# Optimization experiments

Hardware: AMD Instinct MI355X
Metric: run time of the kernel (lower is better)

The kernel has to match this reference:

```python
import jax, jax.numpy as jnp
import numpy as np

B, S, D = 2, 2048, 1024
H_Q, H_KV, DK, DV = 16, 8, 64, 64
R = H_Q // H_KV  # q heads per kv head (GQA)
THETA = 10000.0


def setup_inputs() -> dict:
    key = jax.random.key(0)
    ks = jax.random.split(key, 12)
    inv_freq = 1.0 / (THETA ** (jnp.arange(0, DK, 2, dtype=jnp.float32) / DK))  # [DK/2]
    angles = jnp.arange(S, dtype=jnp.float32)[:, None] * inv_freq[None, :]      # [S, DK/2]
    scale = 0.02
    return {
        "x": jax.random.normal(ks[0], (B, S, D), jnp.float32),
        "Wq": jax.random.normal(ks[1], (D, H_Q * DK), jnp.float32) * scale,
        "bq": jnp.zeros((H_Q * DK,), jnp.float32),
        "Wk": jax.random.normal(ks[2], (D, H_KV * DK), jnp.float32) * scale,
        "bk": jnp.zeros((H_KV * DK,), jnp.float32),
        "Wv": jax.random.normal(ks[3], (D, H_KV * DV), jnp.float32) * scale,
        "bv": jnp.zeros((H_KV * DV,), jnp.float32),
        "Wo": jax.random.normal(ks[4], (H_Q * DV, D), jnp.float32) * scale,
        "bo": jnp.zeros((D,), jnp.float32),
        "freqs_cos": jnp.cos(angles),
        "freqs_sin": jnp.sin(angles),
        "attention_mask": jax.random.bernoulli(ks[5], 0.9, (B, S)),  # True = real token
    }


def _rope(t, cos, sin):
    # t: [B, S, H, Dh]; cos/sin: [S, Dh/2]. Complex rotation on interleaved pairs.
    tp = t.reshape(*t.shape[:-1], -1, 2)
    x1, x2 = tp[..., 0], tp[..., 1]
    c = cos[None, :, None, :]
    s = sin[None, :, None, :]
    o1 = x1 * c - x2 * s
    o2 = x1 * s + x2 * c
    return jnp.stack([o1, o2], axis=-1).reshape(t.shape)


def reference(x, Wq, bq, Wk, bk, Wv, bv, Wo, bo, freqs_cos, freqs_sin, attention_mask):
    b, s, _ = x.shape
    q = (x @ Wq + bq).reshape(b, s, H_Q, DK)
    k = (x @ Wk + bk).reshape(b, s, H_KV, DK)
    v = (x @ Wv + bv).reshape(b, s, H_KV, DV)
    q = _rope(q, freqs_cos, freqs_sin)
    k = _rope(k, freqs_cos, freqs_sin)
    q = q.transpose(0, 2, 1, 3)                      # [B, Hq, S, DK]
    k = jnp.repeat(k.transpose(0, 2, 1, 3), R, axis=1)  # GQA expand -> [B, Hq, S, DK]
    v = jnp.repeat(v.transpose(0, 2, 1, 3), R, axis=1)  # [B, Hq, S, DV]
    causal = jnp.tril(jnp.ones((s, s), dtype=bool))
    # Module does logical_or(padding, causal) -- replicated faithfully.
    mask = jnp.logical_or(attention_mask[:, None, None, :], causal[None, None])
    scale = 1.0 / jnp.sqrt(jnp.float32(DK))
    scores = jnp.einsum('bhqd,bhkd->bhqk', q, k) * scale
    scores = jnp.where(mask, scores, -jnp.inf)
    attn = jax.nn.softmax(scores, axis=-1)
    out = jnp.einsum('bhqk,bhkd->bhqd', attn, v)
    out = out.transpose(0, 2, 1, 3).reshape(b, s, H_Q * DV)
    return out @ Wo + bo
```

## Files before the change

### kernel.cpp

```cpp
#include <hip/hip_runtime.h>
#include <hip/hip_bf16.h>
#include <math.h>

typedef __attribute__((ext_vector_type(8))) short bf16x8;
typedef __attribute__((ext_vector_type(4))) float f32x4;

#define OFF_XB  0ull
#define OFF_WT  (8ull<<20)
#define OFF_WO  (12ull<<20)
#define OFF_QB  (14ull<<20)
#define OFF_KB  (22ull<<20)
#define OFF_VT  (26ull<<20)
#define OFF_AO  (30ull<<20)
#define OFF_MB  (38ull<<20)

#define QSCALE 0.18033688056680276f

__device__ inline unsigned pack_bf162(float a, float b) {
    __hip_bfloat162 t = __float22bfloat162_rn(make_float2(a, b));
    return *(unsigned*)&t;
}

__device__ inline float exp2_fast(float x) {
    float r;
    asm("v_exp_f32 %0, %1" : "=v"(r) : "v"(x));
    return r;
}

__device__ inline void gload16(const void* g, void* l) {
    __builtin_amdgcn_global_load_lds(
        (const __attribute__((address_space(1))) void*)g,
        (__attribute__((address_space(3))) void*)l, 16, 0, 0);
}

__launch_bounds__(256)
__global__ void prep_kernel(const float* __restrict__ x,
                            const float* __restrict__ Wq, const float* __restrict__ Wk,
                            const float* __restrict__ Wv, const float* __restrict__ Wo,
                            const void* __restrict__ mraw,
                            __hip_bfloat16* __restrict__ XB,
                            __hip_bfloat16* __restrict__ WT,
                            __hip_bfloat16* __restrict__ WoT,
                            float* __restrict__ mbias) {
    __shared__ float T[32][33];
    __shared__ int bad01, badf;
    const int tid = threadIdx.x;
    const int bid = blockIdx.x;
    if (bid < 1024) {
        const int base = bid * 4096;
#pragma unroll
        for (int i = 0; i < 4; ++i) {
            const int e = base + (i * 256 + tid) * 4;
            const float4 v = *(const float4*)&x[e];
            uint2 pk;
            pk.x = pack_bf162(v.x, v.y);
            pk.y = pack_bf162(v.z, v.w);
            *(uint2*)&XB[e] = pk;
        }
    } else if (bid < 4096) {
        const float* src; int ldn, nbase; __hip_bfloat16* dst; int n0, k0;
        if (bid < 3072) {
            const int tb = bid - 1024;
            const int kt = tb >> 6, nt = tb & 63;
            n0 = nt * 32; k0 = kt * 32; dst = WT;
            if (n0 < 1024)      { src = Wq; ldn = 1024; nbase = n0; }
            else if (n0 < 1536) { src = Wk; ldn = 512;  nbase = n0 - 1024; }
            else                { src = Wv; ldn = 512;  nbase = n0 - 1536; }
        } else {
            const int tb = bid - 3072;
            const int kt = tb >> 5, nt = tb & 31;
            n0 = nt * 32; k0 = kt * 32; dst = WoT;
            src = Wo; ldn = 1024; nbase = n0;
        }
        const int c = tid & 31, r0 = tid >> 5;
#pragma unroll
        for (int i = 0; i < 4; ++i)
            T[r0 + 8 * i][c] = src[(size_t)(k0 + r0 + 8 * i) * ldn + nbase + c];
        __syncthreads();
#pragma unroll
        for (int i = 0; i < 4; ++i) {
            const int nn = r0 + 8 * i;
            dst[(size_t)(n0 + nn) * 1024 + k0 + c] = __float2bfloat16(T[c][nn]);
        }
    } else {
        if (tid == 0) { bad01 = 0; badf = 0; }
        __syncthreads();
        const unsigned* w = (const unsigned*)mraw;
#pragma unroll
        for (int i = 0; i < 4; ++i) {
            const unsigned v = w[tid * 4 + i];
            if (v > 1u) atomicAdd(&bad01, 1);
            if (v != 0u && v != 0x3F800000u) atomicAdd(&badf, 1);
        }
        __syncthreads();
        const int fmt = (bad01 == 0) ? 0 : ((badf == 0) ? 1 : 2);
        for (int i = tid; i < 4096; i += 256) {
            bool on;
            if (fmt == 2) on = (((const unsigned char*)mraw)[i] != 0);
            else          on = (w[i] != 0u);
            mbias[i] = on ? 0.f : -1e30f;
        }
    }
}

#define QSTAGE(SEL, K0_) do {                                                    \
    _Pragma("unroll") for (int rnd_ = 0; rnd_ < 4; ++rnd_) {                     \
        const int off_ = rnd_ * 4096 + wid * 1024 + lane * 16;                   \
        const int row_ = off_ >> 7;                                              \
        const int ch_  = ((off_ >> 4) & 7) ^ (row_ & 7);                         \
        gload16((const char*)Ag + ((size_t)(n0 + row_) * 1024 + (K0_) + ch_ * 8) * 2, \
                Asm + (SEL) * 16384 + rnd_ * 4096 + wid * 1024);                 \
        gload16((const char*)Bg + ((size_t)(m0 + row_) * 1024 + (K0_) + ch_ * 8) * 2, \
                Bsm + (SEL) * 16384 + rnd_ * 4096 + wid * 1024);                 \
    }                                                                            \
} while (0)

__launch_bounds__(256)
__global__ void qkv_mfma_kernel(const __hip_bfloat16* __restrict__ XB,
                                const __hip_bfloat16* __restrict__ WT,
                                const float* __restrict__ bq, const float* __restrict__ bk,
                                const float* __restrict__ bv,
                                const float* __restrict__ fc, const float* __restrict__ fs,
                                __hip_bfloat16* __restrict__ QB,
                                __hip_bfloat16* __restrict__ KB,
                                __hip_bfloat16* __restrict__ VT) {
    __shared__ __attribute__((aligned(16))) char Asm[32768];
    __shared__ __attribute__((aligned(16))) char Bsm[32768];
    const int tid = threadIdx.x;
    const int lane = tid & 63, wid = tid >> 6;
    const int c = lane & 15, g = lane >> 4;
    const int n0 = blockIdx.x * 128, m0 = blockIdx.y * 128;
    const int wn = (wid >> 1) * 64, wm = (wid & 1) * 64;
    const __hip_bfloat16* Ag = WT;
    const __hip_bfloat16* Bg = XB;

    f32x4 acc[4][4];
#pragma unroll
    for (int ni = 0; ni < 4; ++ni)
#pragma unroll
        for (int mj = 0; mj < 4; ++mj) acc[ni][mj] = f32x4{0.f, 0.f, 0.f, 0.f};

    QSTAGE(0, 0);
    int cur = 0;
    for (int kt = 0; kt < 16; ++kt) {
        const int k0 = kt * 64;
        if (kt < 15) {
            QSTAGE(cur ^ 1, k0 + 64);
            asm volatile("s_waitcnt vmcnt(8)" ::: "memory");
        } else {
            asm volatile("s_waitcnt vmcnt(0)" ::: "memory");
        }
        __builtin_amdgcn_sched_barrier(0);
        __builtin_amdgcn_s_barrier();
        __builtin_amdgcn_sched_barrier(0);

        const char* Ac = Asm + cur * 16384;
        const char* Bc = Bsm + cur * 16384;
#pragma unroll
        for (int ks = 0; ks < 2; ++ks) {
            bf16x8 af[4], bfr[4];
#pragma unroll
            for (int t = 0; t < 4; ++t) {
                const int sl = ((g + 4 * ks) ^ (c & 7)) << 4;
                af[t]  = *(const bf16x8*)(Ac + (wn + 16 * t + c) * 128 + sl);
                bfr[t] = *(const bf16x8*)(Bc + (wm + 16 * t + c) * 128 + sl);
            }
#pragma unroll
            for (int ni = 0; ni < 4; ++ni)
#pragma unroll
                for (int mj = 0; mj < 4; ++mj)
                    acc[ni][mj] = __builtin_amdgcn_mfma_f32_16x16x32_bf16(
                        af[ni], bfr[mj], acc[ni][mj], 0, 0, 0);
        }
        __builtin_amdgcn_sched_barrier(0);
        __builtin_amdgcn_s_barrier();
        __builtin_amdgcn_sched_barrier(0);
        cur ^= 1;
    }

#pragma unroll
    for (int ni = 0; ni < 4; ++ni) {
        const int nb = n0 + wn + 16 * ni + 4 * g;
        const float* bias; int nloc;
        if (nb < 1024)      { bias = bq; nloc = nb; }
        else if (nb < 1536) { bias = bk; nloc = nb - 1024; }
        else                { bias = bv; nloc = nb - 1536; }
        const float4 b4 = *(const float4*)&bias[nloc];
        const int h = nloc >> 6, dk = nb & 63;
#pragma unroll
        for (int mj = 0; mj < 4; ++mj) {
            const int tok = m0 + wm + 16 * mj + c;
            const int bb = tok >> 11, sp = tok & 2047;
            float v0 = acc[ni][mj][0] + b4.x;
            float v1 = acc[ni][mj][1] + b4.y;
            float v2 = acc[ni][mj][2] + b4.z;
            float v3 = acc[ni][mj][3] + b4.w;
            if (nb < 1536) {
                const int p = sp * 32 + (dk >> 1);
                const float c0 = fc[p], s0 = fs[p];
                const float c1 = fc[p + 1], s1 = fs[p + 1];
                float o0 = v0 * c0 - v1 * s0, o1 = v0 * s0 + v1 * c0;
                float o2 = v2 * c1 - v3 * s1, o3 = v2 * s1 + v3 * c1;
                uint2 pk;
                if (nb < 1024) {
                    o0 *= QSCALE; o1 *= QSCALE; o2 *= QSCALE; o3 *= QSCALE;
                    pk.x = pack_bf162(o0, o1); pk.y = pack_bf162(o2, o3);
                    *(uint2*)&QB[(size_t)((bb * 16 + h) * 2048 + sp) * 64 + dk] = pk;
                } else {
                    pk.x = pack_bf162(o0, o1); pk.y = pack_bf162(o2, o3);
                    *(uint2*)&KB[(size_t)((bb * 8 + h) * 2048 + sp) * 64 + dk] = pk;
                }
            } else {
                const size_t vb = (size_t)((bb * 8 + h) * 64 + dk) * 2048 + sp;
                VT[vb]          = __float2bfloat16(v0);
                VT[vb + 2048]   = __float2bfloat16(v1);
                VT[vb + 4096]   = __float2bfloat16(v2);
                VT[vb + 6144]   = __float2bfloat16(v3);
            }
        }
    }
}

__launch_bounds__(256)
__global__ void out_mfma_kernel(const __hip_bfloat16* __restrict__ AOB,
                                const __hip_bfloat16* __restrict__ WoT,
                                const float* __restrict__ bo,
                                float* __restrict__ out) {
    __shared__ __attribute__((aligned(16))) char Asm[32768];
    __shared__ __attribute__((aligned(16))) char Bsm[32768];
    const int tid = threadIdx.x;
    const int lane = tid & 63, wid = tid >> 6;
    const int c = lane & 15, g = lane >> 4;
    const int n0 = blockIdx.x * 128, m0 = blockIdx.y * 128;
    const int wn = (wid >> 1) * 64, wm = (wid & 1) * 64;
    const __hip_bfloat16* Ag = WoT;
    const __hip_bfloat16* Bg = AOB;

    f32x4 acc[4][4];
#pragma unroll
    for (int ni = 0; ni < 4; ++ni)
#pragma unroll
        for (int mj = 0; mj < 4; ++mj) acc[ni][mj] = f32x4{0.f, 0.f, 0.f, 0.f};

    QSTAGE(0, 0);
    int cur = 0;
    for (int kt = 0; kt < 16; ++kt) {
        const int k0 = kt * 64;
        if (kt < 15) {
            QSTAGE(cur ^ 1, k0 + 64);
            asm volatile("s_waitcnt vmcnt(8)" ::: "memory");
        } else {
            asm volatile("s_waitcnt vmcnt(0)" ::: "memory");
        }
        __builtin_amdgcn_sched_barrier(0);
        __builtin_amdgcn_s_barrier();
        __builtin_amdgcn_sched_barrier(0);

        const char* Ac = Asm + cur * 16384;
        const char* Bc = Bsm + cur * 16384;
#pragma unroll
        for (int ks = 0; ks < 2; ++ks) {
            bf16x8 af[4], bfr[4];
#pragma unroll
            for (int t = 0; t < 4; ++t) {
                const int sl = ((g + 4 * ks) ^ (c & 7)) << 4;
                af[t]  = *(const bf16x8*)(Ac + (wn + 16 * t + c) * 128 + sl);
                bfr[t] = *(const bf16x8*)(Bc + (wm + 16 * t + c) * 128 + sl);
            }
#pragma unroll
            for (int ni = 0; ni < 4; ++ni)
#pragma unroll
                for (int mj = 0; mj < 4; ++mj)
                    acc[ni][mj] = __builtin_amdgcn_mfma_f32_16x16x32_bf16(
                        af[ni], bfr[mj], acc[ni][mj], 0, 0, 0);
        }
        __builtin_amdgcn_sched_barrier(0);
        __builtin_amdgcn_s_barrier();
        __builtin_amdgcn_sched_barrier(0);
        cur ^= 1;
    }
#pragma unroll
    for (int ni = 0; ni < 4; ++ni) {
        const int nb = n0 + wn + 16 * ni + 4 * g;
        const float4 b4 = *(const float4*)&bo[nb];
#pragma unroll
        for (int mj = 0; mj < 4; ++mj) {
            const int tok = m0 + wm + 16 * mj + c;
            const f32x4 a = acc[ni][mj];
            const float4 st = make_float4(a[0] + b4.x, a[1] + b4.y,
                                          a[2] + b4.z, a[3] + b4.w);
            *(float4*)&out[(size_t)tok * 1024 + nb] = st;
        }
    }
}


#define STAGE128(SEL, K0_) do {                                                  \
    _Pragma("unroll") for (int rnd_ = 0; rnd_ < 4; ++rnd_) {                     \
        const int off_ = rnd_ * 4096 + wid * 1024 + lane * 16;                   \
        const int kr_ = off_ >> 7;                                               \
        const int kc_ = ((off_ >> 4) & 7) ^ (kr_ & 7);                           \
        gload16(Kh + (size_t)((K0_) + kr_) * 64 + kc_ * 8,                       \
                Ksm + (SEL) * 16384 + rnd_ * 4096 + wid * 1024);                 \
        const int vr_ = off_ >> 8;                                               \
        const int vc_ = ((off_ >> 4) & 15) ^ (vr_ & 15);                         \
        gload16(Vh + (size_t)vr_ * 2048 + (K0_) + vc_ * 8,                       \
                Vsm + (SEL) * 16384 + rnd_ * 4096 + wid * 1024);                 \
    }                                                                            \
} while (0)

__launch_bounds__(256, 2)
__global__ void attn_kernel(const __hip_bfloat16* __restrict__ QB,
                            const __hip_bfloat16* __restrict__ KB,
                            const __hip_bfloat16* __restrict__ VT,
                            const float* __restrict__ maskb,
                            __hip_bfloat16* __restrict__ AOB) {
    __shared__ __attribute__((aligned(16))) char Ksm[32768];
    __shared__ __attribute__((aligned(16))) char Vsm[32768];
    __shared__ char P_lds[4][4096];

    const int tid  = threadIdx.x;
    const int lane = tid & 63, wid = tid >> 6;
    const int c = lane & 15, g = lane >> 4;

    const int bid = blockIdx.x;
    const int o_  = (bid & 7) * 64 + (bid >> 3);
    const int qx = o_ & 15, h = (o_ >> 4) & 15, b = o_ >> 8;
    const int qb = qx * 128 + wid * 32;

    const __hip_bfloat16* Qh = QB + (size_t)(b * 16 + h)       * 2048 * 64;
    const __hip_bfloat16* Kh = KB + (size_t)(b * 8 + (h >> 1)) * 2048 * 64;
    const __hip_bfloat16* Vh = VT + (size_t)(b * 8 + (h >> 1)) * 64 * 2048;
    const float* mb = maskb + b * 2048;

    STAGE128(0, 0);

    bf16x8 bq[2][2];
#pragma unroll
    for (int rt = 0; rt < 2; ++rt)
#pragma unroll
        for (int ks = 0; ks < 2; ++ks)
            bq[rt][ks] = *(const bf16x8*)&Qh[(size_t)(qb + 16 * rt + c) * 64
                                             + 32 * ks + 8 * g];
    __syncthreads();

    const short oneb = (short)0x3F80;
    const bf16x8 ones = {oneb, oneb, oneb, oneb, oneb, oneb, oneb, oneb};

    f32x4 o[2][4];
    f32x4 lacc[2];
#pragma unroll
    for (int rt = 0; rt < 2; ++rt) {
        lacc[rt] = f32x4{0.f, 0.f, 0.f, 0.f};
#pragma unroll
        for (int mt = 0; mt < 4; ++mt) o[rt][mt] = f32x4{0.f, 0.f, 0.f, 0.f};
    }
    float m_[2] = {-INFINITY, -INFINITY};

    char* Pr = &P_lds[wid][0] + c * 256;
    const int swz = (c & 7) << 4;

    int cur = 0;
    for (int kt = 0; kt < 16; ++kt) {
        const int k0 = kt * 128;
        if (kt < 15) {
            STAGE128(cur ^ 1, k0 + 128);
            asm volatile("s_waitcnt vmcnt(8)" ::: "memory");
        } else {
            asm volatile("s_waitcnt vmcnt(0)" ::: "memory");
        }
        __builtin_amdgcn_sched_barrier(0);
        __builtin_amdgcn_s_barrier();
        __builtin_amdgcn_sched_barrier(0);

        const char* Kc = Ksm + cur * 16384;
        const char* Vc = Vsm + cur * 16384;

        const bool needb = (k0 + 127 > qb);
        f32x4 bv4[8];
        if (needb) {
#pragma unroll
            for (int mt = 0; mt < 8; ++mt)
                bv4[mt] = *(const f32x4*)&mb[k0 + 16 * mt + 4 * g];
        }

        f32x4 st[2][8];
        __builtin_amdgcn_s_setprio(1);
#pragma unroll
        for (int hf = 0; hf < 2; ++hf) {
            bf16x8 ak[4][2];
#pragma unroll
            for (int mt = 0; mt < 4; ++mt)
#pragma unroll
                for (int ks = 0; ks < 2; ++ks)
                    ak[mt][ks] = *(const bf16x8*)(Kc + (64 * hf + 16 * mt + c) * 128
                                                  + (((g + 4 * ks) ^ (c & 7)) << 4));
#pragma unroll
            for (int rt = 0; rt < 2; ++rt)
#pragma unroll
                for (int mt = 0; mt < 4; ++mt) {
                    f32x4 z = f32x4{0.f, 0.f, 0.f, 0.f};
                    z = __builtin_amdgcn_mfma_f32_16x16x32_bf16(ak[mt][0], bq[rt][0], z, 0, 0, 0);
                    z = __builtin_amdgcn_mfma_f32_16x16x32_bf16(ak[mt][1], bq[rt][1], z, 0, 0, 0);
                    st[rt][4 * hf + mt] = z;
                }
        }
        __builtin_amdgcn_s_setprio(0);

#pragma unroll
        for (int rt = 0; rt < 2; ++rt) {
            const int qw = qb + 16 * rt;
            if (k0 + 127 <= qw) {
            } else if (k0 > qw + 15) {
#pragma unroll
                for (int mt = 0; mt < 8; ++mt)
                    st[rt][mt] = st[rt][mt] + bv4[mt];
            } else {
                const int qg = qw + c;
#pragma unroll
                for (int mt = 0; mt < 8; ++mt)
#pragma unroll
                    for (int r = 0; r < 4; ++r) {
                        const int kg = k0 + 16 * mt + 4 * g + r;
                        st[rt][mt][r] += (kg <= qg) ? 0.f : bv4[mt][r];
                    }
            }
            const f32x4 a0 = __builtin_elementwise_max(st[rt][0], st[rt][1]);
            const f32x4 a1 = __builtin_elementwise_max(st[rt][2], st[rt][3]);
            const f32x4 a2 = __builtin_elementwise_max(st[rt][4], st[rt][5]);
            const f32x4 a3 = __builtin_elementwise_max(st[rt][6], st[rt][7]);
            const f32x4 b0 = __builtin_elementwise_max(a0, a1);
            const f32x4 b1 = __builtin_elementwise_max(a2, a3);
            const f32x4 mv = __builtin_elementwise_max(b0, b1);
            float pmax = fmaxf(fmaxf(mv[0], mv[1]), fmaxf(mv[2], mv[3]));
            pmax = fmaxf(pmax, __shfl_xor(pmax, 16));
            pmax = fmaxf(pmax, __shfl_xor(pmax, 32));
            if (!__all(pmax <= m_[rt] + 11.5f)) {
                const float mn = fmaxf(m_[rt], pmax);
                const float alpha = exp2_fast(m_[rt] - mn);
                m_[rt] = mn;
                lacc[rt][0] *= alpha;
#pragma unroll
                for (int mt = 0; mt < 4; ++mt) o[rt][mt] *= alpha;
            }
            const float mneg = m_[rt];
            const f32x4 m4 = {mneg, mneg, mneg, mneg};
#pragma unroll
            for (int mt = 0; mt < 8; ++mt) {
                const f32x4 e = st[rt][mt] - m4;
#pragma unroll
                for (int r = 0; r < 4; ++r)
                    st[rt][mt][r] = exp2_fast(e[r]);
            }

#pragma unroll
            for (int mt = 0; mt < 8; ++mt) {
                const unsigned w0 = pack_bf162(st[rt][mt][0], st[rt][mt][1]);
                const unsigned w1 = pack_bf162(st[rt][mt][2], st[rt][mt][3]);
                *(unsigned long long*)(Pr + ((32 * mt + 8 * g) ^ swz)) =
                    (unsigned long long)w0 | ((unsigned long long)w1 << 32);
            }

            __builtin_amdgcn_s_setprio(1);
#pragma unroll
            for (int ks = 0; ks < 4; ++ks) {
                const bf16x8 pb = *(const bf16x8*)(Pr + ((64 * ks + 16 * g) ^ swz));
                bf16x8 av[4];
#pragma unroll
                for (int mt = 0; mt < 4; ++mt)
                    av[mt] = *(const bf16x8*)(Vc + (16 * mt + c) * 256
                                              + (((4 * ks + g) ^ (c & 15)) << 4));
#pragma unroll
                for (int mt = 0; mt < 4; ++mt)
                    o[rt][mt] = __builtin_amdgcn_mfma_f32_16x16x32_bf16(av[mt], pb, o[rt][mt], 0, 0, 0);
                lacc[rt] = __builtin_amdgcn_mfma_f32_16x16x32_bf16(ones, pb, lacc[rt], 0, 0, 0);
            }
            __builtin_amdgcn_s_setprio(0);
        }

        __builtin_amdgcn_sched_barrier(0);
        __builtin_amdgcn_s_barrier();
        __builtin_amdgcn_sched_barrier(0);
        cur ^= 1;
    }

#pragma unroll
    for (int rt = 0; rt < 2; ++rt) {
        const float inv = 1.f / lacc[rt][0];
        const size_t tok = (size_t)(b * 2048 + qb + 16 * rt + c);
#pragma unroll
        for (int mt = 0; mt < 4; ++mt) {
            uint2 pk;
            pk.x = pack_bf162(o[rt][mt][0] * inv, o[rt][mt][1] * inv);
            pk.y = pack_bf162(o[rt][mt][2] * inv, o[rt][mt][3] * inv);
            *(uint2*)&AOB[tok * 1024 + h * 64 + 16 * mt + 4 * g] = pk;
        }
    }
}

extern "C" void kernel_launch(void* const* d_in, const int* in_sizes, int n_in,
                              void* d_out, int out_size, void* d_ws, size_t ws_size,
                              hipStream_t stream) {
    const float* x  = (const float*)d_in[0];
    const float* Wq = (const float*)d_in[1];
    const float* bq = (const float*)d_in[2];
    const float* Wk = (const float*)d_in[3];
    const float* bk = (const float*)d_in[4];
    const float* Wv = (const float*)d_in[5];
    const float* bv = (const float*)d_in[6];
    const float* Wo = (const float*)d_in[7];
    const float* bo = (const float*)d_in[8];
    const float* fc = (const float*)d_in[9];
    const float* fs = (const float*)d_in[10];
    const void*  am = d_in[11];

    char* ws = (char*)d_ws;
    __hip_bfloat16* XB  = (__hip_bfloat16*)(ws + OFF_XB);
    __hip_bfloat16* WT  = (__hip_bfloat16*)(ws + OFF_WT);
    __hip_bfloat16* WoT = (__hip_bfloat16*)(ws + OFF_WO);
    __hip_bfloat16* QB  = (__hip_bfloat16*)(ws + OFF_QB);
    __hip_bfloat16* KB  = (__hip_bfloat16*)(ws + OFF_KB);
    __hip_bfloat16* VT  = (__hip_bfloat16*)(ws + OFF_VT);
    __hip_bfloat16* AOB = (__hip_bfloat16*)(ws + OFF_AO);
    float* mbias = (float*)(ws + OFF_MB);
    float* out   = (float*)d_out;

    hipLaunchKernelGGL(prep_kernel, dim3(4097), dim3(256), 0, stream,
                       x, Wq, Wk, Wv, Wo, am, XB, WT, WoT, mbias);
    hipLaunchKernelGGL(qkv_mfma_kernel, dim3(16, 32), dim3(256), 0, stream,
                       XB, WT, bq, bk, bv, fc, fs, QB, KB, VT);
    hipLaunchKernelGGL(attn_kernel, dim3(512), dim3(256), 0, stream,
                       QB, KB, VT, mbias, AOB);
    hipLaunchKernelGGL(out_mfma_kernel, dim3(8, 32), dim3(256), 0, stream,
                       AOB, WoT, bo, out);
}
```

Measured before the change: 132.0 us.

## Software-pipeline attention so QK of next tile overlaps softmax/PV of previous

```diff
diff --git a/kernel.cpp b/kernel.cpp
--- a/kernel.cpp
+++ b/kernel.cpp
@@ -295,17 +295,105 @@
 }
 
 
-#define STAGE128(SEL, K0_) do {                                                  \
+#define STAGE_K(SEL, T_) do {                                                    \
+    const int sk0_ = (T_) * 128;                                                 \
     _Pragma("unroll") for (int rnd_ = 0; rnd_ < 4; ++rnd_) {                     \
         const int off_ = rnd_ * 4096 + wid * 1024 + lane * 16;                   \
         const int kr_ = off_ >> 7;                                               \
         const int kc_ = ((off_ >> 4) & 7) ^ (kr_ & 7);                           \
-        gload16(Kh + (size_t)((K0_) + kr_) * 64 + kc_ * 8,                       \
+        gload16(Kh + (size_t)(sk0_ + kr_) * 64 + kc_ * 8,                        \
                 Ksm + (SEL) * 16384 + rnd_ * 4096 + wid * 1024);                 \
+    }                                                                            \
+} while (0)
+
+#define STAGE_V(SEL, T_) do {                                                    \
+    const int sv0_ = (T_) * 128;                                                 \
+    _Pragma("unroll") for (int rnd_ = 0; rnd_ < 4; ++rnd_) {                     \
+        const int off_ = rnd_ * 4096 + wid * 1024 + lane * 16;                   \
         const int vr_ = off_ >> 8;                                               \
         const int vc_ = ((off_ >> 4) & 15) ^ (vr_ & 15);                         \
-        gload16(Vh + (size_t)vr_ * 2048 + (K0_) + vc_ * 8,                       \
+        gload16(Vh + (size_t)vr_ * 2048 + sv0_ + vc_ * 8,                        \
                 Vsm + (SEL) * 16384 + rnd_ * 4096 + wid * 1024);                 \
+    }                                                                            \
+} while (0)
+
+#define SOFTMAX_PV(PT, VC_) do {                                                 \
+    const int kp0_ = (PT) * 128;                                                 \
+    _Pragma("unroll") for (int rt = 0; rt < 2; ++rt) {                           \
+        const int qw_ = qb + 16 * rt;                                            \
+        if (kp0_ + 127 <= qw_) {                                                 \
+        } else if (kp0_ > qw_ + 15) {                                            \
+            _Pragma("unroll") for (int mt = 0; mt < 8; ++mt)                     \
+                stp[rt][mt] = stp[rt][mt] + bv4[mt];                             \
+        } else {                                                                 \
+            const int qg_ = qw_ + c;                                             \
+            _Pragma("unroll") for (int mt = 0; mt < 8; ++mt)                     \
+            _Pragma("unroll") for (int r = 0; r < 4; ++r) {                      \
+                const int kg_ = kp0_ + 16 * mt + 4 * g + r;                      \
+                stp[rt][mt][r] += (kg_ <= qg_) ? 0.f : bv4[mt][r];               \
+            }                                                                    \
+        }                                                                        \
+        const f32x4 a0_ = __builtin_elementwise_max(stp[rt][0], stp[rt][1]);     \
+        const f32x4 a1_ = __builtin_elementwise_max(stp[rt][2], stp[rt][3]);     \
+        const f32x4 a2_ = __builtin_elementwise_max(stp[rt][4], stp[rt][5]);     \
+        const f32x4 a3_ = __builtin_elementwise_max(stp[rt][6], stp[rt][7]);     \
+        const f32x4 b0_ = __builtin_elementwise_max(a0_, a1_);                   \
+        const f32x4 b1_ = __builtin_elementwise_max(a2_, a3_);                   \
+        const f32x4 mv_ = __builtin_elementwise_max(b0_, b1_);                   \
+        float pmax = fmaxf(fmaxf(mv_[0], mv_[1]), fmaxf(mv_[2], mv_[3]));        \
+        pmax = fmaxf(pmax, __shfl_xor(pmax, 16));                                \
+        pmax = fmaxf(pmax, __shfl_xor(pmax, 32));                                \
+        if (!__all(pmax <= m_[rt] + 11.5f)) {                                    \
+            const float mn_ = fmaxf(m_[rt], pmax);                               \
+            const float alpha_ = exp2_fast(m_[rt] - mn_);                        \
+            m_[rt] = mn_;                                                        \
+            lacc[rt][0] *= alpha_;                                               \
+            _Pragma("unroll") for (int mt = 0; mt < 4; ++mt) o[rt][mt] *= alpha_;\
+        }                                                                        \
+        const f32x4 m4_ = {m_[rt], m_[rt], m_[rt], m_[rt]};                      \
+        _Pragma("unroll") for (int mt = 0; mt < 8; ++mt) {                       \
+            const f32x4 e_ = stp[rt][mt] - m4_;                                  \
+            _Pragma("unroll") for (int r = 0; r < 4; ++r)                        \
+                stp[rt][mt][r] = exp2_fast(e_[r]);                               \
+        }                                                                        \
+        _Pragma("unroll") for (int mt = 0; mt < 8; ++mt) {                       \
+            const unsigned w0_ = pack_bf162(stp[rt][mt][0], stp[rt][mt][1]);     \
+            const unsigned w1_ = pack_bf162(stp[rt][mt][2], stp[rt][mt][3]);     \
+            *(unsigned long long*)(Pr + ((32 * mt + 8 * g) ^ swz)) =             \
+                (unsigned long long)w0_ | ((unsigned long long)w1_ << 32);       \
+        }                                                                        \
+        _Pragma("unroll") for (int ks = 0; ks < 4; ++ks) {                       \
+            const bf16x8 pb_ = *(const bf16x8*)(Pr + ((64 * ks + 16 * g) ^ swz));\
+            bf16x8 av_[4];                                                       \
+            _Pragma("unroll") for (int mt = 0; mt < 4; ++mt)                     \
+                av_[mt] = *(const bf16x8*)((VC_) + (16 * mt + c) * 256           \
+                                           + (((4 * ks + g) ^ (c & 15)) << 4));  \
+            _Pragma("unroll") for (int mt = 0; mt < 4; ++mt)                     \
+                o[rt][mt] = __builtin_amdgcn_mfma_f32_16x16x32_bf16(             \
+                    av_[mt], pb_, o[rt][mt], 0, 0, 0);                           \
+            lacc[rt] = __builtin_amdgcn_mfma_f32_16x16x32_bf16(                  \
+                ones, pb_, lacc[rt], 0, 0, 0);                                   \
+        }                                                                        \
+    }                                                                            \
+} while (0)
+
+#define QK_TILE(DST, T_) do {                                                    \
+    const char* Kc_ = Ksm + ((T_) & 1) * 16384;                                  \
+    _Pragma("unroll") for (int hf = 0; hf < 2; ++hf) {                           \
+        bf16x8 ak_[4][2];                                                        \
+        _Pragma("unroll") for (int mt = 0; mt < 4; ++mt)                         \
+        _Pragma("unroll") for (int ks = 0; ks < 2; ++ks)                         \
+            ak_[mt][ks] = *(const bf16x8*)(Kc_ + (64 * hf + 16 * mt + c) * 128   \
+                                           + (((g + 4 * ks) ^ (c & 7)) << 4));   \
+        _Pragma("unroll") for (int rt = 0; rt < 2; ++rt)                         \
+        _Pragma("unroll") for (int mt = 0; mt < 4; ++mt) {                       \
+            f32x4 z_ = f32x4{0.f, 0.f, 0.f, 0.f};                                \
+            z_ = __builtin_amdgcn_mfma_f32_16x16x32_bf16(ak_[mt][0], bq[rt][0],  \
+                                                         z_, 0, 0, 0);           \
+            z_ = __builtin_amdgcn_mfma_f32_16x16x32_bf16(ak_[mt][1], bq[rt][1],  \
+                                                         z_, 0, 0, 0);           \
+            DST[rt][4 * hf + mt] = z_;                                           \
+        }                                                                        \
     }                                                                            \
 } while (0)
 
@@ -333,8 +421,7 @@
     const __hip_bfloat16* Vh = VT + (size_t)(b * 8 + (h >> 1)) * 64 * 2048;
     const float* mb = maskb + b * 2048;
 
-    STAGE128(0, 0);
-
+    STAGE_K(0, 0);
     bf16x8 bq[2][2];
 #pragma unroll
     for (int rt = 0; rt < 2; ++rt)
@@ -360,128 +447,54 @@
     char* Pr = &P_lds[wid][0] + c * 256;
     const int swz = (c & 7) << 4;
 
-    int cur = 0;
-    for (int kt = 0; kt < 16; ++kt) {
-        const int k0 = kt * 128;
-        if (kt < 15) {
-            STAGE128(cur ^ 1, k0 + 128);
-            asm volatile("s_waitcnt vmcnt(8)" ::: "memory");
-        } else {
-            asm volatile("s_waitcnt vmcnt(0)" ::: "memory");
-        }
+    f32x4 stp[2][8], stc[2][8];
+    STAGE_K(1, 1);
+    STAGE_V(0, 0);
+    QK_TILE(stp, 0);
+
+    for (int t = 1; t < 16; ++t) {
+        asm volatile("s_waitcnt vmcnt(0)" ::: "memory");
         __builtin_amdgcn_sched_barrier(0);
         __builtin_amdgcn_s_barrier();
         __builtin_amdgcn_sched_barrier(0);
 
-        const char* Kc = Ksm + cur * 16384;
-        const char* Vc = Vsm + cur * 16384;
-
-        const bool needb = (k0 + 127 > qb);
+        const int p = t - 1;
+        const int kp0 = p * 128;
         f32x4 bv4[8];
-        if (needb) {
+        if (kp0 + 127 > qb) {
 #pragma unroll
             for (int mt = 0; mt < 8; ++mt)
-                bv4[mt] = *(const f32x4*)&mb[k0 + 16 * mt + 4 * g];
-        }
-
-        f32x4 st[2][8];
-        __builtin_amdgcn_s_setprio(1);
-#pragma unroll
-        for (int hf = 0; hf < 2; ++hf) {
-            bf16x8 ak[4][2];
-#pragma unroll
-            for (int mt = 0; mt < 4; ++mt)
-#pragma unroll
-                for (int ks = 0; ks < 2; ++ks)
-                    ak[mt][ks] = *(const bf16x8*)(Kc + (64 * hf + 16 * mt + c) * 128
-                                                  + (((g + 4 * ks) ^ (c & 7)) << 4));
-#pragma unroll
-            for (int rt = 0; rt < 2; ++rt)
-#pragma unroll
-                for (int mt = 0; mt < 4; ++mt) {
-                    f32x4 z = f32x4{0.f, 0.f, 0.f, 0.f};
-                    z = __builtin_amdgcn_mfma_f32_16x16x32_bf16(ak[mt][0], bq[rt][0], z, 0, 0, 0);
-                    z = __builtin_amdgcn_mfma_f32_16x16x32_bf16(ak[mt][1], bq[rt][1], z, 0, 0, 0);
-                    st[rt][4 * hf + mt] = z;
-                }
-        }
-        __builtin_amdgcn_s_setprio(0);
-
-#pragma unroll
-        for (int rt = 0; rt < 2; ++rt) {
-            const int qw = qb + 16 * rt;
-            if (k0 + 127 <= qw) {
-            } else if (k0 > qw + 15) {
-#pragma unroll
-                for (int mt = 0; mt < 8; ++mt)
-                    st[rt][mt] = st[rt][mt] + bv4[mt];
-            } else {
-                const int qg = qw + c;
-#pragma unroll
-                for (int mt = 0; mt < 8; ++mt)
-#pragma unroll
-                    for (int r = 0; r < 4; ++r) {
-                        const int kg = k0 + 16 * mt + 4 * g + r;
-                        st[rt][mt][r] += (kg <= qg) ? 0.f : bv4[mt][r];
-                    }
-            }
-            const f32x4 a0 = __builtin_elementwise_max(st[rt][0], st[rt][1]);
-            const f32x4 a1 = __builtin_elementwise_max(st[rt][2], st[rt][3]);
-            const f32x4 a2 = __builtin_elementwise_max(st[rt][4], st[rt][5]);
-            const f32x4 a3 = __builtin_elementwise_max(st[rt][6], st[rt][7]);
-            const f32x4 b0 = __builtin_elementwise_max(a0, a1);
-            const f32x4 b1 = __builtin_elementwise_max(a2, a3);
-            const f32x4 mv = __builtin_elementwise_max(b0, b1);
-            float pmax = fmaxf(fmaxf(mv[0], mv[1]), fmaxf(mv[2], mv[3]));
-            pmax = fmaxf(pmax, __shfl_xor(pmax, 16));
-            pmax = fmaxf(pmax, __shfl_xor(pmax, 32));
-            if (!__all(pmax <= m_[rt] + 11.5f)) {
-                const float mn = fmaxf(m_[rt], pmax);
-                const float alpha = exp2_fast(m_[rt] - mn);
-                m_[rt] = mn;
-                lacc[rt][0] *= alpha;
-#pragma unroll
-                for (int mt = 0; mt < 4; ++mt) o[rt][mt] *= alpha;
-            }
-            const float mneg = m_[rt];
-            const f32x4 m4 = {mneg, mneg, mneg, mneg};
-#pragma unroll
-            for (int mt = 0; mt < 8; ++mt) {
-                const f32x4 e = st[rt][mt] - m4;
-#pragma unroll
-                for (int r = 0; r < 4; ++r)
-                    st[rt][mt][r] = exp2_fast(e[r]);
-            }
-
-#pragma unroll
-            for (int mt = 0; mt < 8; ++mt) {
-                const unsigned w0 = pack_bf162(st[rt][mt][0], st[rt][mt][1]);
-                const unsigned w1 = pack_bf162(st[rt][mt][2], st[rt][mt][3]);
-                *(unsigned long long*)(Pr + ((32 * mt + 8 * g) ^ swz)) =
-                    (unsigned long long)w0 | ((unsigned long long)w1 << 32);
-            }
-
-            __builtin_amdgcn_s_setprio(1);
-#pragma unroll
-            for (int ks = 0; ks < 4; ++ks) {
-                const bf16x8 pb = *(const bf16x8*)(Pr + ((64 * ks + 16 * g) ^ swz));
-                bf16x8 av[4];
-#pragma unroll
-                for (int mt = 0; mt < 4; ++mt)
-                    av[mt] = *(const bf16x8*)(Vc + (16 * mt + c) * 256
-                                              + (((4 * ks + g) ^ (c & 15)) << 4));
-#pragma unroll
-                for (int mt = 0; mt < 4; ++mt)
-                    o[rt][mt] = __builtin_amdgcn_mfma_f32_16x16x32_bf16(av[mt], pb, o[rt][mt], 0, 0, 0);
-                lacc[rt] = __builtin_amdgcn_mfma_f32_16x16x32_bf16(ones, pb, lacc[rt], 0, 0, 0);
-            }
-            __builtin_amdgcn_s_setprio(0);
-        }
+                bv4[mt] = *(const f32x4*)&mb[kp0 + 16 * mt + 4 * g];
+        }
+        if (t < 15) STAGE_K((t + 1) & 1, t + 1);
+        STAGE_V(t & 1, t);
+
+        QK_TILE(stc, t);
+        SOFTMAX_PV(p, Vsm + (p & 1) * 16384);
 
         __builtin_amdgcn_sched_barrier(0);
         __builtin_amdgcn_s_barrier();
         __builtin_amdgcn_sched_barrier(0);
-        cur ^= 1;
+
+#pragma unroll
+        for (int rt = 0; rt < 2; ++rt)
+#pragma unroll
+            for (int mt = 0; mt < 8; ++mt) stp[rt][mt] = stc[rt][mt];
+    }
+
+    asm volatile("s_waitcnt vmcnt(0)" ::: "memory");
+    __builtin_amdgcn_sched_barrier(0);
+    __builtin_amdgcn_s_barrier();
+    __builtin_amdgcn_sched_barrier(0);
+    {
+        const int kp0 = 15 * 128;
+        f32x4 bv4[8];
+        if (kp0 + 127 > qb) {
+#pragma unroll
+            for (int mt = 0; mt < 8; ++mt)
+                bv4[mt] = *(const f32x4*)&mb[kp0 + 16 * mt + 4 * g];
+        }
+        SOFTMAX_PV(15, Vsm + 16384);
     }
 
 #pragma unroll
```

Measured after the change: 154.8 us. 17.3% more time.
